# Optimization experiments

Hardware: AMD Instinct MI355X
Metric: run time of the kernel (lower is better)

## Reference

```python
import jax, jax.numpy as jnp
import numpy as np

NBITS = 8
QMAX = 2 ** (NBITS - 1) - 1  # 127
EPS_S = 1e-8


def ste_round(x):
    # straight-through estimator round (matches HAWQ ste_round)
    return x + jax.lax.stop_gradient(jnp.round(x) - x)


def quant_act(x):
    # symmetric per-tensor 8-bit fake quantization (QuantAct)
    s = jnp.maximum(jnp.max(jnp.abs(x)) / QMAX, EPS_S)
    xq = jnp.clip(ste_round(x / s), -QMAX - 1, QMAX)
    return xq * s, s


def quant_weight_per_channel(w, axis=0):
    # symmetric per-output-channel 8-bit fake quantization (weights)
    red = tuple(i for i in range(w.ndim) if i != axis)
    s = jnp.maximum(jnp.max(jnp.abs(w), axis=red, keepdims=True) / QMAX, EPS_S)
    wq = jnp.clip(ste_round(w / s), -QMAX - 1, QMAX)
    return wq * s, s


def setup_inputs() -> dict:
    key = jax.random.key(0)
    ks = jax.random.split(key, 6)
    B, Cin, Cout, H, W = 32, 256, 128, 56, 56
    x = jax.random.normal(ks[0], (B, Cin, H, W), jnp.float32)
    bn_gamma = 1.0 + 0.1 * jax.random.normal(ks[1], (Cin,), jnp.float32)
    bn_beta = 0.1 * jax.random.normal(ks[2], (Cin,), jnp.float32)
    bn_mean = 0.1 * jax.random.normal(ks[3], (Cin,), jnp.float32)
    bn_var = jax.random.uniform(ks[4], (Cin,), jnp.float32, minval=0.5, maxval=1.5)
    conv_w = jax.random.normal(ks[5], (Cout, Cin), jnp.float32) * (1.0 / np.sqrt(Cin))
    return {"x": x, "bn_gamma": bn_gamma, "bn_beta": bn_beta,
            "bn_mean": bn_mean, "bn_var": bn_var, "conv_w": conv_w}


def reference(x, bn_gamma, bn_beta, bn_mean, bn_var, conv_w):
    bn_eps = 1e-5
    # --- QuantAct on incoming activations ---
    x, act_s = quant_act(x)
    # --- QuantBn: fold BN into per-channel scale/shift, quantize folded weight ---
    w_fold = bn_gamma * jax.lax.rsqrt(bn_var + bn_eps)        # [Cin]
    b_fold = bn_beta - bn_mean * w_fold                       # [Cin]
    wq, bn_s = quant_weight_per_channel(w_fold, axis=0)
    x = x * wq[None, :, None, None] + b_fold[None, :, None, None]
    # --- QuantAct1: requantize post-BN output (act_s * bn_s threaded) ---
    x, act_s = quant_act(x)
    # --- ReLU ---
    x = jax.nn.relu(x)
    # --- QuantConv2d: 1x1 conv, per-output-channel quantized weight ---
    cwq, conv_s = quant_weight_per_channel(conv_w, axis=0)    # [Cout, Cin]
    x = jnp.einsum('bchw,oc->bohw', x, cwq)                   # [B, Cout, H, W]
    # --- QuantAct2: requantize post-conv output ---
    x, act_s = quant_act(x)
    # --- QuantAveragePool2d(2,2): pool in integer domain, rescale back ---
    B, C, H, W = x.shape
    x_int = x / act_s
    pooled = x_int.reshape(B, C, H // 2, 2, W // 2, 2).mean(axis=(3, 5))
    x = pooled * act_s
    # --- QuantAct3 ---
    x, act_s = quant_act(x)
    return x, act_s
```

## Files before the change

### kernel.cpp

```cpp
#include <hip/hip_runtime.h>
#include <math.h>

#define QMAXF 127.0f
#define EPSF  1e-8f
#define CIN   256
#define COUT  128
#define HW    3136
#define W_    56
#define NPOOL 3211264
#define POOL_BLOCKS 1792

typedef unsigned short u16;
typedef unsigned int   u32;
typedef __attribute__((ext_vector_type(8))) short s16x8;
typedef __attribute__((ext_vector_type(4))) float f32x4;

#define WQ_OFF   8
#define BF_OFF   264
#define EMAX_OFF 520
#define EMIN_OFF 776
#define CS_OFF   1032
#define CSS2_OFF 1160
#define CWB_OFF  1288
#define LUT_OFF  17672
#define Y_OFF    50440

__device__ __forceinline__ float qclip(float v) {
    return fminf(fmaxf(v, -128.0f), 127.0f);
}
__device__ __forceinline__ u16 bf16bits(float f) {
    return (u16)(__float_as_uint(f) >> 16);
}
__device__ __forceinline__ u32 encf(float f) {
    u32 u = __float_as_uint(f);
    return (u & 0x80000000u) ? ~u : (u | 0x80000000u);
}
__device__ __forceinline__ float decf(u32 k) {
    return __uint_as_float((k & 0x80000000u) ? (k ^ 0x80000000u) : ~k);
}

__device__ __forceinline__ void block_max_atomic(float v, float* red, u32* dst) {
    #pragma unroll
    for (int off = 32; off > 0; off >>= 1) v = fmaxf(v, __shfl_xor(v, off));
    const int lane = threadIdx.x & 63, wid = threadIdx.x >> 6;
    if (lane == 0) red[wid] = v;
    __syncthreads();
    if (threadIdx.x == 0) {
        const int nw = blockDim.x >> 6;
        float m = red[0];
        for (int i = 1; i < nw; ++i) m = fmaxf(m, red[i]);
        atomicMax(dst, __float_as_uint(m));
    }
}

__global__ void k0w(const float* __restrict__ cw, float* __restrict__ ws) {
    const int t = threadIdx.x;
    if (blockIdx.x == COUT) {
        ((u32*)ws)[EMAX_OFF + t] = 0u;
        ((u32*)ws)[EMIN_OFF + t] = 0xFFFFFFFFu;
        if (t < 2) ((u32*)ws)[2 + t] = 0u;
        return;
    }
    __shared__ float red[4];
    const int o = blockIdx.x;
    const float wv = cw[o * CIN + t];
    float v = fabsf(wv);
    #pragma unroll
    for (int off = 32; off > 0; off >>= 1) v = fmaxf(v, __shfl_xor(v, off));
    if ((t & 63) == 0) red[t >> 6] = v;
    __syncthreads();
    const float mx = fmaxf(fmaxf(red[0], red[1]), fmaxf(red[2], red[3]));
    const float s = fmaxf(mx / QMAXF, EPSF);
    const float q = qclip(rintf(wv / s));
    ((u16*)(ws + CWB_OFF))[o * CIN + t] = bf16bits(q);
    if (t == 0) ws[CS_OFF + o] = s;
}

__global__ void k1_minmax(const float* __restrict__ x, float* __restrict__ ws) {
    __shared__ float red[8];
    const int row = blockIdx.x;
    const float4* xr = (const float4*)(x + (size_t)row * HW);
    float mx = -3.402823466e38f, mn = 3.402823466e38f;
    for (int i = threadIdx.x; i < HW / 4; i += 256) {
        const float4 v = xr[i];
        mx = fmaxf(mx, fmaxf(fmaxf(v.x, v.y), fmaxf(v.z, v.w)));
        mn = fminf(mn, fminf(fminf(v.x, v.y), fminf(v.z, v.w)));
    }
    #pragma unroll
    for (int off = 32; off > 0; off >>= 1) {
        mx = fmaxf(mx, __shfl_xor(mx, off));
        mn = fminf(mn, __shfl_xor(mn, off));
    }
    if ((threadIdx.x & 63) == 0) {
        red[threadIdx.x >> 6] = mx;
        red[4 + (threadIdx.x >> 6)] = mn;
    }
    __syncthreads();
    if (threadIdx.x == 0) {
        mx = fmaxf(fmaxf(red[0], red[1]), fmaxf(red[2], red[3]));
        mn = fminf(fminf(red[4], red[5]), fminf(red[6], red[7]));
        const int c = row & (CIN - 1);
        atomicMax((u32*)ws + EMAX_OFF + c, encf(mx));
        atomicMin((u32*)ws + EMIN_OFF + c, encf(mn));
    }
}

__global__ void k0b(const float* __restrict__ g, const float* __restrict__ be,
                    const float* __restrict__ mnp, const float* __restrict__ vr,
                    float* __restrict__ ws) {
    __shared__ float red[4];
    __shared__ float s1sh;
    const int t = threadIdx.x;
    const float cmax = decf(((u32*)ws)[EMAX_OFF + t]);
    const float cmin = decf(((u32*)ws)[EMIN_OFF + t]);
    float v = fmaxf(fabsf(cmax), fabsf(cmin));
    #pragma unroll
    for (int off = 32; off > 0; off >>= 1) v = fmaxf(v, __shfl_xor(v, off));
    if ((t & 63) == 0) red[t >> 6] = v;
    __syncthreads();
    if (t == 0) {
        const float m1 = fmaxf(fmaxf(red[0], red[1]), fmaxf(red[2], red[3]));
        ws[0] = m1;
        s1sh = fmaxf(m1 / QMAXF, EPSF);
    }
    __syncthreads();
    const float s1 = s1sh;
    const float wf = g[t] / sqrtf(vr[t] + 1e-5f);
    const float bf = be[t] - mnp[t] * wf;
    const float sw = fmaxf(fabsf(wf) / QMAXF, EPSF);
    const float q  = qclip(rintf(wf / sw));
    const float wqd = __fmul_rn(q, sw);
    ws[WQ_OFF + t] = wqd;
    ws[BF_OFF + t] = bf;
    const float q1h = qclip(rintf(cmax / s1));
    const float q1l = qclip(rintf(cmin / s1));
    const float xh = __fadd_rn(__fmul_rn(__fmul_rn(q1h, s1), wqd), bf);
    const float xl = __fadd_rn(__fmul_rn(__fmul_rn(q1l, s1), wqd), bf);
    float m2 = fmaxf(fabsf(xh), fabsf(xl));
    __syncthreads();
    #pragma unroll
    for (int off = 32; off > 0; off >>= 1) m2 = fmaxf(m2, __shfl_xor(m2, off));
    if ((t & 63) == 0) red[t >> 6] = m2;
    __syncthreads();
    if (t == 0) ws[1] = fmaxf(fmaxf(red[0], red[1]), fmaxf(red[2], red[3]));
}

__global__ void k0L(float* __restrict__ ws) {
    const int c = blockIdx.x;
    const int t = threadIdx.x;
    const float s1 = fmaxf(ws[0] / QMAXF, EPSF);
    const float s2 = fmaxf(ws[1] / QMAXF, EPSF);
    const float wqd = ws[WQ_OFF + c];
    const float bf  = ws[BF_OFF + c];
    const float q1f = (float)(t - 127);
    const float xd  = __fmul_rn(q1f, s1);
    const float x2  = __fadd_rn(__fmul_rn(xd, wqd), bf);
    const float q2  = qclip(rintf(x2 / s2));
    const float a   = fmaxf(q2, 0.0f);
    ((u16*)(ws + LUT_OFF))[(c << 8) + t] = bf16bits(a);
    if (c == 0 && t < COUT)
        ws[CSS2_OFF + t] = __fmul_rn(s2, ws[CS_OFF + t]);
}

__device__ __forceinline__ void stage32(u16* __restrict__ Xs, u16* __restrict__ Wt,
                                        const float* __restrict__ xr,
                                        const s16x8* __restrict__ wreg,
                                        int t, int ck, float s1,
                                        const u16* __restrict__ lut) {
    const int p = t & 31, kh = t >> 5;
    u32 pk[4];
    #pragma unroll
    for (int jj = 0; jj < 4; ++jj) {
        const int c0 = ck + kh * 8 + 2 * jj;
        const float q1a = rintf(xr[2 * jj] / s1);
        const float q1b = rintf(xr[2 * jj + 1] / s1);
        const u32 lo = lut[(c0 << 8) + 127 + (int)q1a];
        const u32 hi = lut[((c0 + 1) << 8) + 127 + (int)q1b];
        pk[jj] = lo | (hi << 16);
    }
    uint4 v; v.x = pk[0]; v.y = pk[1]; v.z = pk[2]; v.w = pk[3];
    *(uint4*)&Xs[p * 64 + (((kh + p + (p >> 3)) & 7) * 8)] = v;
    #pragma unroll
    for (int ps = 0; ps < 4; ++ps) {
        const int o = ps * 32 + (t >> 3);
        *(s16x8*)&Wt[o * 64 + ((((t & 7) + o + (o >> 3)) & 7) * 8)] = wreg[ps];
    }
}

__global__ __launch_bounds__(256) void k3_mfma(const float* __restrict__ x,
                                               float* __restrict__ ws) {
    __shared__ __align__(16) u16 Xs[32 * 64];
    __shared__ __align__(16) u16 Wt[128 * 64];
    __shared__ float Css2s[COUT];
    __shared__ float red[4];

    const int t   = threadIdx.x;
    const int b   = blockIdx.x / 98;
    const int hw0 = (blockIdx.x % 98) * 32;
    const int l   = t & 63, w = t >> 6;
    const int wc  = w * 32;

    const float s1 = fmaxf(ws[0] / QMAXF, EPSF);
    const u16* lut = (const u16*)(ws + LUT_OFF);
    const u16* cwb = (const u16*)(ws + CWB_OFF);

    if (t < COUT) Css2s[t] = ws[CSS2_OFF + t];

    const int p  = t & 31;
    const int kh = t >> 5;
    const float* xb = x + (size_t)b * CIN * HW + hw0 + p;

    float xr[8];
    s16x8 wreg[4];

    #pragma unroll
    for (int ps = 0; ps < 4; ++ps)
        wreg[ps] = *(const s16x8*)(cwb + (ps * 32 + (t >> 3)) * CIN + (t & 7) * 8);
    #pragma unroll
    for (int j = 0; j < 8; ++j)
        xr[j] = xb[(kh * 8 + j) * HW];

    f32x4 acc[2][2];
    #pragma unroll
    for (int m = 0; m < 2; ++m)
        #pragma unroll
        for (int n = 0; n < 2; ++n) acc[m][n] = (f32x4)0.0f;

    stage32(Xs, Wt, xr, wreg, t, 0, s1, lut);
    __syncthreads();

    #pragma unroll
    for (int it = 0; it < 4; ++it) {
        const int ckn = (it + 1) * 64;
        if (it < 3) {
            #pragma unroll
            for (int ps = 0; ps < 4; ++ps)
                wreg[ps] = *(const s16x8*)(cwb + (ps * 32 + (t >> 3)) * CIN + ckn + (t & 7) * 8);
            #pragma unroll
            for (int j = 0; j < 8; ++j)
                xr[j] = xb[(ckn + kh * 8 + j) * HW];
        }
        #pragma unroll
        for (int ks = 0; ks < 2; ++ks) {
            const int ch = ks * 4 + (l >> 4);
            s16x8 xf[2], wfr[2];
            #pragma unroll
            for (int n = 0; n < 2; ++n) {
                const int pp = n * 16 + (l & 15);
                xf[n] = *(const s16x8*)&Xs[pp * 64 + (((ch + pp + (pp >> 3)) & 7) * 8)];
            }
            #pragma unroll
            for (int m = 0; m < 2; ++m) {
                const int o = wc + m * 16 + (l & 15);
                wfr[m] = *(const s16x8*)&Wt[o * 64 + (((ch + o + (o >> 3)) & 7) * 8)];
            }
            #pragma unroll
            for (int m = 0; m < 2; ++m)
                #pragma unroll
                for (int n = 0; n < 2; ++n)
                    acc[m][n] = __builtin_amdgcn_mfma_f32_16x16x32_bf16(
                                    wfr[m], xf[n], acc[m][n], 0, 0, 0);
        }
        if (it < 3) {
            __syncthreads();
            stage32(Xs, Wt, xr, wreg, t, ckn, s1, lut);
            __syncthreads();
        }
    }

    float mloc = 0.0f;
    #pragma unroll
    for (int m = 0; m < 2; ++m) {
        #pragma unroll
        for (int n = 0; n < 2; ++n) {
            const int pix = hw0 + n * 16 + (l & 15);
            #pragma unroll
            for (int r = 0; r < 4; ++r) {
                const int o = wc + m * 16 + (l >> 4) * 4 + r;
                const float val = __fmul_rn(acc[m][n][r], Css2s[o]);
                ws[Y_OFF + ((size_t)(b * COUT + o)) * HW + pix] = val;
                mloc = fmaxf(mloc, fabsf(val));
            }
        }
    }
    block_max_atomic(mloc, red, (u32*)ws + 2);
}

__global__ void k4_pool(float* __restrict__ ws, float* __restrict__ out) {
    __shared__ float red[4];
    const float s3 = fmaxf(ws[2] / QMAXF, EPSF);
    float mloc = 0.0f;
    const int nq2 = NPOOL / 2;
    for (int pp = blockIdx.x * 256 + threadIdx.x; pp < nq2;
         pp += POOL_BLOCKS * 256) {
        const int j2  = pp % 14;
        const int tmp = pp / 14;
        const int i   = tmp % 28;
        const int bo  = tmp / 28;
        const float* yb = ws + Y_OFF + (size_t)bo * HW + (2 * i) * W_ + 4 * j2;
        const float4 r0 = *(const float4*)yb;
        const float4 r1 = *(const float4*)(yb + W_);
        const float q00 = qclip(rintf(r0.x / s3)), q01 = qclip(rintf(r0.y / s3));
        const float q02 = qclip(rintf(r0.z / s3)), q03 = qclip(rintf(r0.w / s3));
        const float q10 = qclip(rintf(r1.x / s3)), q11 = qclip(rintf(r1.y / s3));
        const float q12 = qclip(rintf(r1.z / s3)), q13 = qclip(rintf(r1.w / s3));
        const float p0 = __fmul_rn(__fmul_rn((q00 + q01) + (q10 + q11), 0.25f), s3);
        const float p1 = __fmul_rn(__fmul_rn((q02 + q03) + (q12 + q13), 0.25f), s3);
        float2 pv; pv.x = p0; pv.y = p1;
        *(float2*)(out + (size_t)bo * 784 + i * 28 + 2 * j2) = pv;
        mloc = fmaxf(mloc, fmaxf(fabsf(p0), fabsf(p1)));
    }
    block_max_atomic(mloc, red, (u32*)ws + 3);
}

__global__ void k5_final(float* __restrict__ out, const float* __restrict__ ws) {
    const float s4 = fmaxf(ws[3] / QMAXF, EPSF);
    const int n4 = NPOOL / 4;
    for (int i = blockIdx.x * 256 + threadIdx.x; i < n4; i += 3136 * 256) {
        float4 v = *(float4*)(out + 4 * (size_t)i);
        v.x = __fmul_rn(qclip(rintf(v.x / s4)), s4);
        v.y = __fmul_rn(qclip(rintf(v.y / s4)), s4);
        v.z = __fmul_rn(qclip(rintf(v.z / s4)), s4);
        v.w = __fmul_rn(qclip(rintf(v.w / s4)), s4);
        *(float4*)(out + 4 * (size_t)i) = v;
    }
    if (blockIdx.x == 0 && threadIdx.x == 0) out[NPOOL] = s4;
}

extern "C" void kernel_launch(void* const* d_in, const int* in_sizes, int n_in,
                              void* d_out, int out_size, void* d_ws, size_t ws_size,
                              hipStream_t stream) {
    const float* x     = (const float*)d_in[0];
    const float* gamma = (const float*)d_in[1];
    const float* beta  = (const float*)d_in[2];
    const float* mean  = (const float*)d_in[3];
    const float* var   = (const float*)d_in[4];
    const float* cw    = (const float*)d_in[5];
    float* out = (float*)d_out;
    float* ws  = (float*)d_ws;

    hipLaunchKernelGGL(k0w, dim3(COUT + 1), dim3(256), 0, stream, cw, ws);
    hipLaunchKernelGGL(k1_minmax, dim3(32 * CIN), dim3(256), 0, stream, x, ws);
    hipLaunchKernelGGL(k0b, dim3(1), dim3(256), 0, stream, gamma, beta, mean, var, ws);
    hipLaunchKernelGGL(k0L, dim3(256), dim3(256), 0, stream, ws);
    hipLaunchKernelGGL(k3_mfma, dim3(3136), dim3(256), 0, stream, x, ws);
    hipLaunchKernelGGL(k4_pool, dim3(POOL_BLOCKS), dim3(256), 0, stream, ws, out);
    hipLaunchKernelGGL(k5_final, dim3(3136), dim3(256), 0, stream, out, ws);
}
```

Baseline: 119.4 us.

## Split conv into LUT transform pass and double-buffered direct-to-LDS MFMA GEMM

Moves activation quantization and the BN/ReLU lookup out of the GEMM kernel into a separate pass that writes a pre-swizzled bf16 activation image. The conv weights are likewise stored pre-swizzled, so the GEMM can copy tiles straight from global memory into LDS with global_load_lds and double buffering. Each GEMM block now handles 64 pixels with a 4x2 MFMA tile per wave, and the output is stored in a blocked layout that the pool kernel indexes. This removes per-element conversion and staging stalls from the GEMM loop, but adds a full write and read of an intermediate bf16 tensor plus an extra kernel launch.

```diff
diff --git a/kernel.cpp b/kernel.cpp
--- a/kernel.cpp
+++ b/kernel.cpp
@@ -21,9 +21,9 @@
 #define EMIN_OFF 776
 #define CS_OFF   1032
 #define CSS2_OFF 1160
-#define CWB_OFF  1288
-#define LUT_OFF  17672
-#define Y_OFF    50440
+#define LUT_OFF  1288
+#define WIMG_OFF 34056
+#define A_OFF    50440
 
 __device__ __forceinline__ float qclip(float v) {
     return fminf(fmaxf(v, -128.0f), 127.0f);
@@ -37,6 +37,11 @@
 }
 __device__ __forceinline__ float decf(u32 k) {
     return __uint_as_float((k & 0x80000000u) ? (k ^ 0x80000000u) : ~k);
+}
+__device__ __forceinline__ void gload16(const u16* g, u16* l) {
+    __builtin_amdgcn_global_load_lds((const __attribute__((address_space(1))) u32*)g,
+                                     (__attribute__((address_space(3))) u32*)l,
+                                     16, 0, 0);
 }
 
 __device__ __forceinline__ void block_max_atomic(float v, float* red, u32* dst) {
@@ -72,7 +77,9 @@
     const float mx = fmaxf(fmaxf(red[0], red[1]), fmaxf(red[2], red[3]));
     const float s = fmaxf(mx / QMAXF, EPSF);
     const float q = qclip(rintf(wv / s));
-    ((u16*)(ws + CWB_OFF))[o * CIN + t] = bf16bits(q);
+    const int ckt = t >> 6, kloc = t & 63, koct = kloc >> 3, klow = kloc & 7;
+    ((u16*)(ws + WIMG_OFF))[ckt * 8192 + o * 64 +
+                            ((koct + o + (o >> 3)) & 7) * 8 + klow] = bf16bits(q);
     if (t == 0) ws[CS_OFF + o] = s;
 }
 
@@ -162,123 +169,129 @@
         ws[CSS2_OFF + t] = __fmul_rn(s2, ws[CS_OFF + t]);
 }
 
-__device__ __forceinline__ void stage32(u16* __restrict__ Xs, u16* __restrict__ Wt,
-                                        const float* __restrict__ xr,
-                                        const s16x8* __restrict__ wreg,
-                                        int t, int ck, float s1,
-                                        const u16* __restrict__ lut) {
-    const int p = t & 31, kh = t >> 5;
-    u32 pk[4];
-    #pragma unroll
-    for (int jj = 0; jj < 4; ++jj) {
-        const int c0 = ck + kh * 8 + 2 * jj;
-        const float q1a = rintf(xr[2 * jj] / s1);
-        const float q1b = rintf(xr[2 * jj + 1] / s1);
-        const u32 lo = lut[(c0 << 8) + 127 + (int)q1a];
-        const u32 hi = lut[((c0 + 1) << 8) + 127 + (int)q1b];
-        pk[jj] = lo | (hi << 16);
-    }
-    uint4 v; v.x = pk[0]; v.y = pk[1]; v.z = pk[2]; v.w = pk[3];
-    *(uint4*)&Xs[p * 64 + (((kh + p + (p >> 3)) & 7) * 8)] = v;
-    #pragma unroll
-    for (int ps = 0; ps < 4; ++ps) {
-        const int o = ps * 32 + (t >> 3);
-        *(s16x8*)&Wt[o * 64 + ((((t & 7) + o + (o >> 3)) & 7) * 8)] = wreg[ps];
-    }
-}
-
-__global__ __launch_bounds__(256) void k3_mfma(const float* __restrict__ x,
-                                               float* __restrict__ ws) {
-    __shared__ __align__(16) u16 Xs[32 * 64];
-    __shared__ __align__(16) u16 Wt[128 * 64];
+__global__ __launch_bounds__(256) void kA_xform(const float* __restrict__ x,
+                                                float* __restrict__ ws) {
+    const int t = threadIdx.x;
+    const int b = blockIdx.x / 49, t64 = blockIdx.x % 49;
+    const int hw0 = t64 * 64;
+    const int pl = t & 63, kh16 = t >> 6;
+    const float s1 = fmaxf(ws[0] / QMAXF, EPSF);
+    const u16* lut = (const u16*)(ws + LUT_OFF);
+    u16* A16 = (u16*)(ws + A_OFF);
+    const int swa = ((kh16 * 2 + pl + (pl >> 3)) & 7) * 8;
+    const int swb = ((kh16 * 2 + 1 + pl + (pl >> 3)) & 7) * 8;
+    #pragma unroll
+    for (int ckt = 0; ckt < 4; ++ckt) {
+        const int c0 = ckt * 64 + kh16 * 16;
+        const float* xb = x + ((size_t)(b * CIN + c0)) * HW + hw0 + pl;
+        float xv[16];
+        #pragma unroll
+        for (int j = 0; j < 16; ++j) xv[j] = xb[j * HW];
+        u32 pk[8];
+        #pragma unroll
+        for (int jj = 0; jj < 8; ++jj) {
+            const int q1a = (int)rintf(xv[2 * jj] / s1);
+            const int q1b = (int)rintf(xv[2 * jj + 1] / s1);
+            const u32 lo = lut[((c0 + 2 * jj) << 8) + 127 + q1a];
+            const u32 hi = lut[((c0 + 2 * jj + 1) << 8) + 127 + q1b];
+            pk[jj] = lo | (hi << 16);
+        }
+        u16* slab = A16 + ((((size_t)(b * 49 + t64)) * 4 + ckt) << 12) + pl * 64;
+        uint4 v0; v0.x = pk[0]; v0.y = pk[1]; v0.z = pk[2]; v0.w = pk[3];
+        uint4 v1; v1.x = pk[4]; v1.y = pk[5]; v1.z = pk[6]; v1.w = pk[7];
+        *(uint4*)(slab + swa) = v0;
+        *(uint4*)(slab + swb) = v1;
+    }
+}
+
+__global__ __launch_bounds__(256) void kB_gemm(float* __restrict__ ws) {
+    __shared__ __align__(16) u16 Xl[2][4096];
+    __shared__ __align__(16) u16 Wl[2][8192];
     __shared__ float Css2s[COUT];
     __shared__ float red[4];
 
-    const int t   = threadIdx.x;
-    const int b   = blockIdx.x / 98;
-    const int hw0 = (blockIdx.x % 98) * 32;
-    const int l   = t & 63, w = t >> 6;
-    const int wc  = w * 32;
-
-    const float s1 = fmaxf(ws[0] / QMAXF, EPSF);
-    const u16* lut = (const u16*)(ws + LUT_OFF);
-    const u16* cwb = (const u16*)(ws + CWB_OFF);
+    const int t = threadIdx.x;
+    const int b = blockIdx.x / 49, t64 = blockIdx.x % 49;
+    const int l = t & 63, w = t >> 6;
+    const int wc = (w >> 1) * 64;
+    const int wp = (w & 1) * 32;
+
+    const u16* A16 = (const u16*)(ws + A_OFF);
+    const u16* W16 = (const u16*)(ws + WIMG_OFF);
+    const size_t slab0 = ((size_t)(b * 49 + t64)) << 14;
 
     if (t < COUT) Css2s[t] = ws[CSS2_OFF + t];
 
-    const int p  = t & 31;
-    const int kh = t >> 5;
-    const float* xb = x + (size_t)b * CIN * HW + hw0 + p;
-
-    float xr[8];
-    s16x8 wreg[4];
-
-    #pragma unroll
-    for (int ps = 0; ps < 4; ++ps)
-        wreg[ps] = *(const s16x8*)(cwb + (ps * 32 + (t >> 3)) * CIN + (t & 7) * 8);
-    #pragma unroll
-    for (int j = 0; j < 8; ++j)
-        xr[j] = xb[(kh * 8 + j) * HW];
-
-    f32x4 acc[2][2];
-    #pragma unroll
-    for (int m = 0; m < 2; ++m)
+    f32x4 acc[4][2];
+    #pragma unroll
+    for (int m = 0; m < 4; ++m)
         #pragma unroll
         for (int n = 0; n < 2; ++n) acc[m][n] = (f32x4)0.0f;
 
-    stage32(Xs, Wt, xr, wreg, t, 0, s1, lut);
+    const int wvb = (t >> 6) * 512;
+    const int tsrc = t * 8;
+
+    {
+        const u16* sX = A16 + slab0;
+        const u16* sW = W16;
+        #pragma unroll
+        for (int r = 0; r < 2; ++r)
+            gload16(sX + tsrc + r * 2048, &Xl[0][wvb + r * 2048]);
+        #pragma unroll
+        for (int r = 0; r < 4; ++r)
+            gload16(sW + tsrc + r * 2048, &Wl[0][wvb + r * 2048]);
+    }
     __syncthreads();
 
     #pragma unroll
     for (int it = 0; it < 4; ++it) {
-        const int ckn = (it + 1) * 64;
+        const int buf = it & 1;
         if (it < 3) {
-            #pragma unroll
-            for (int ps = 0; ps < 4; ++ps)
-                wreg[ps] = *(const s16x8*)(cwb + (ps * 32 + (t >> 3)) * CIN + ckn + (t & 7) * 8);
-            #pragma unroll
-            for (int j = 0; j < 8; ++j)
-                xr[j] = xb[(ckn + kh * 8 + j) * HW];
+            const u16* sX = A16 + slab0 + (size_t)(it + 1) * 4096;
+            const u16* sW = W16 + (it + 1) * 8192;
+            #pragma unroll
+            for (int r = 0; r < 2; ++r)
+                gload16(sX + tsrc + r * 2048, &Xl[buf ^ 1][wvb + r * 2048]);
+            #pragma unroll
+            for (int r = 0; r < 4; ++r)
+                gload16(sW + tsrc + r * 2048, &Wl[buf ^ 1][wvb + r * 2048]);
         }
         #pragma unroll
         for (int ks = 0; ks < 2; ++ks) {
             const int ch = ks * 4 + (l >> 4);
-            s16x8 xf[2], wfr[2];
+            s16x8 xf[2], wfr[4];
             #pragma unroll
             for (int n = 0; n < 2; ++n) {
-                const int pp = n * 16 + (l & 15);
-                xf[n] = *(const s16x8*)&Xs[pp * 64 + (((ch + pp + (pp >> 3)) & 7) * 8)];
+                const int pp = wp + n * 16 + (l & 15);
+                xf[n] = *(const s16x8*)&Xl[buf][pp * 64 + (((ch + pp + (pp >> 3)) & 7) * 8)];
             }
             #pragma unroll
-            for (int m = 0; m < 2; ++m) {
+            for (int m = 0; m < 4; ++m) {
                 const int o = wc + m * 16 + (l & 15);
-                wfr[m] = *(const s16x8*)&Wt[o * 64 + (((ch + o + (o >> 3)) & 7) * 8)];
+                wfr[m] = *(const s16x8*)&Wl[buf][o * 64 + (((ch + o + (o >> 3)) & 7) * 8)];
             }
             #pragma unroll
-            for (int m = 0; m < 2; ++m)
+            for (int m = 0; m < 4; ++m)
                 #pragma unroll
                 for (int n = 0; n < 2; ++n)
                     acc[m][n] = __builtin_amdgcn_mfma_f32_16x16x32_bf16(
                                     wfr[m], xf[n], acc[m][n], 0, 0, 0);
         }
-        if (it < 3) {
-            __syncthreads();
-            stage32(Xs, Wt, xr, wreg, t, ckn, s1, lut);
-            __syncthreads();
-        }
-    }
-
+        __syncthreads();
+    }
+
+    float* yblk = ws + A_OFF + (((size_t)(b * 49 + t64)) << 13);
     float mloc = 0.0f;
     #pragma unroll
-    for (int m = 0; m < 2; ++m) {
+    for (int m = 0; m < 4; ++m) {
         #pragma unroll
         for (int n = 0; n < 2; ++n) {
-            const int pix = hw0 + n * 16 + (l & 15);
+            const int pixl = wp + n * 16 + (l & 15);
             #pragma unroll
             for (int r = 0; r < 4; ++r) {
                 const int o = wc + m * 16 + (l >> 4) * 4 + r;
                 const float val = __fmul_rn(acc[m][n][r], Css2s[o]);
-                ws[Y_OFF + ((size_t)(b * COUT + o)) * HW + pix] = val;
+                yblk[o * 64 + pixl] = val;
                 mloc = fmaxf(mloc, fabsf(val));
             }
         }
@@ -297,18 +310,24 @@
         const int tmp = pp / 14;
         const int i   = tmp % 28;
         const int bo  = tmp / 28;
-        const float* yb = ws + Y_OFF + (size_t)bo * HW + (2 * i) * W_ + 4 * j2;
-        const float4 r0 = *(const float4*)yb;
-        const float4 r1 = *(const float4*)(yb + W_);
+        const int b = bo >> 7, o = bo & 127;
+        const int p0 = (2 * i) * W_ + 4 * j2;
+        const int p1 = p0 + W_;
+        const float* y0 = ws + A_OFF + (((size_t)(b * 49 + (p0 >> 6))) << 13)
+                          + (o << 6) + (p0 & 63);
+        const float* y1 = ws + A_OFF + (((size_t)(b * 49 + (p1 >> 6))) << 13)
+                          + (o << 6) + (p1 & 63);
+        const float4 r0 = *(const float4*)y0;
+        const float4 r1 = *(const float4*)y1;
         const float q00 = qclip(rintf(r0.x / s3)), q01 = qclip(rintf(r0.y / s3));
         const float q02 = qclip(rintf(r0.z / s3)), q03 = qclip(rintf(r0.w / s3));
         const float q10 = qclip(rintf(r1.x / s3)), q11 = qclip(rintf(r1.y / s3));
         const float q12 = qclip(rintf(r1.z / s3)), q13 = qclip(rintf(r1.w / s3));
-        const float p0 = __fmul_rn(__fmul_rn((q00 + q01) + (q10 + q11), 0.25f), s3);
-        const float p1 = __fmul_rn(__fmul_rn((q02 + q03) + (q12 + q13), 0.25f), s3);
-        float2 pv; pv.x = p0; pv.y = p1;
+        const float p0v = __fmul_rn(__fmul_rn((q00 + q01) + (q10 + q11), 0.25f), s3);
+        const float p1v = __fmul_rn(__fmul_rn((q02 + q03) + (q12 + q13), 0.25f), s3);
+        float2 pv; pv.x = p0v; pv.y = p1v;
         *(float2*)(out + (size_t)bo * 784 + i * 28 + 2 * j2) = pv;
-        mloc = fmaxf(mloc, fmaxf(fabsf(p0), fabsf(p1)));
+        mloc = fmaxf(mloc, fmaxf(fabsf(p0v), fabsf(p1v)));
     }
     block_max_atomic(mloc, red, (u32*)ws + 3);
 }
@@ -343,7 +362,8 @@
     hipLaunchKernelGGL(k1_minmax, dim3(32 * CIN), dim3(256), 0, stream, x, ws);
     hipLaunchKernelGGL(k0b, dim3(1), dim3(256), 0, stream, gamma, beta, mean, var, ws);
     hipLaunchKernelGGL(k0L, dim3(256), dim3(256), 0, stream, ws);
-    hipLaunchKernelGGL(k3_mfma, dim3(3136), dim3(256), 0, stream, x, ws);
+    hipLaunchKernelGGL(kA_xform, dim3(1568), dim3(256), 0, stream, x, ws);
+    hipLaunchKernelGGL(kB_gemm, dim3(1568), dim3(256), 0, stream, ws);
     hipLaunchKernelGGL(k4_pool, dim3(POOL_BLOCKS), dim3(256), 0, stream, ws, out);
     hipLaunchKernelGGL(k5_final, dim3(3136), dim3(256), 0, stream, out, ws);
 }
```

Result: slower. 137.0 us (+14.8%).
